# Optimization experiments

Measured on AMD Instinct MI355X. Metric: run time of the kernel, lower is better.

## Reference

```python
import jax, jax.numpy as jnp
import numpy as np

INPUT_WIDTH = 256
DEPTH = 7
OUTPUT_WIDTH = 256
N_NODES = 2 ** (DEPTH + 1) - 1  # 255


def setup_inputs() -> dict:
    key = jax.random.key(0)
    k_x, k_w1, k_w2 = jax.random.split(key, 3)
    init1 = 1.0 / np.sqrt(INPUT_WIDTH)
    x = jax.random.normal(k_x, (2, 1024, INPUT_WIDTH), dtype=jnp.float32)
    w1s = jax.random.uniform(k_w1, (N_NODES, INPUT_WIDTH), jnp.float32, -init1, init1)
    b1s = jnp.zeros((N_NODES,), jnp.float32)
    w2s = jax.random.uniform(k_w2, (N_NODES, INPUT_WIDTH, OUTPUT_WIDTH), jnp.float32, -init1, init1)
    b2s = jnp.zeros((N_NODES, OUTPUT_WIDTH), jnp.float32)
    return {"x": x, "w1s": w1s, "b1s": b1s, "w2s": w2s, "b2s": b2s}


def reference(x, w1s, b1s, w2s, b2s):
    B, S, D = x.shape
    flat_x = x.reshape(B * S, D)  # [T, D]
    T = flat_x.shape[0]

    # --- routing pass: walk the binary tree, recording node ids and logits ---
    current = jnp.zeros((T,), dtype=jnp.int32)
    all_nodes = []
    all_logits = []
    for _ in range(DEPTH + 1):
        all_nodes.append(current)
        score = jnp.einsum('td,td->t', flat_x, w1s[current]) + b1s[current]  # [T]
        all_logits.append(score)
        # ((sign+1)/2).long(): sign(0)->0 maps to choice 0 via truncation
        choice = ((jnp.sign(score) + 1.0) / 2.0).astype(jnp.int32)
        current = current * 2 + choice + 1

    logits = jnp.stack(all_logits, axis=1)  # [T, DEPTH+1]
    path_weights = jax.nn.gelu(jnp.abs(logits), approximate=False)  # exact erf GELU

    # --- output pass: weighted sum of per-node transforms along the path ---
    out = jnp.zeros((T, OUTPUT_WIDTH), dtype=x.dtype)
    for i in range(DEPTH + 1):
        nodes_i = all_nodes[i]
        t_i = jnp.einsum('td,tdo->to', flat_x, w2s[nodes_i]) + b2s[nodes_i]  # [T, O]
        out = out + t_i * path_weights[:, i][:, None]

    return out.reshape(B, S, OUTPUT_WIDTH)
```

## Files before the change

kernel.cpp:

```cpp
#include <hip/hip_runtime.h>
#include <hip/hip_bf16.h>

#define T_TOKENS 2048
#define DIM 256
#define NLEV 8

using bf16x8 = __attribute__((ext_vector_type(8))) short;
using f32x4  = __attribute__((ext_vector_type(4))) float;

__device__ __forceinline__ unsigned short f2bf(float f) {
    union { float f; unsigned u; } v; v.f = f;
    unsigned r = v.u + 0x7FFFu + ((v.u >> 16) & 1u);
    return (unsigned short)(r >> 16);
}

__global__ __launch_bounds__(256) void route_kernel(
    const float* __restrict__ x, const float* __restrict__ w1s,
    const float* __restrict__ b1s,
    float* __restrict__ pw,
    int*   __restrict__ pc,
    unsigned short* __restrict__ xbf)
{
    int wave = threadIdx.x >> 6;
    int lane = threadIdx.x & 63;
    int t = blockIdx.x * 4 + wave;

    const float4 xv = *reinterpret_cast<const float4*>(x + (size_t)t * DIM + lane * 4);

    ushort4 xb;
    xb.x = f2bf(xv.x); xb.y = f2bf(xv.y); xb.z = f2bf(xv.z); xb.w = f2bf(xv.w);
    *reinterpret_cast<ushort4*>(xbf + (size_t)t * DIM + lane * 4) = xb;

    int p = 1;
    float keep = 0.0f;
    #pragma unroll
    for (int lvl = 0; lvl < NLEV; ++lvl) {
        int node = p - 1;
        const float4 wv = *reinterpret_cast<const float4*>(w1s + (size_t)node * DIM + lane * 4);
        float s = xv.x * wv.x + xv.y * wv.y + xv.z * wv.z + xv.w * wv.w;
        #pragma unroll
        for (int off = 32; off; off >>= 1) s += __shfl_xor(s, off);
        float score = s + b1s[node];
        float a = fabsf(score);
        float g = a * 0.5f * (1.0f + erff(a * 0.70710678118654752f));
        if (lane == lvl) keep = g;
        int choice = (score > 0.0f) ? 1 : 0;
        p = 2 * p + choice;
    }
    if (lane < NLEV) pw[(size_t)t * NLEV + lane] = keep;
    if (lane == 0) pc[t] = p;
}

__global__ __launch_bounds__(256) void sort_kernel(
    const int* __restrict__ pc,
    int* __restrict__ order, unsigned* __restrict__ units, int* __restrict__ ucount)
{
    __shared__ int hist[256];
    __shared__ int offs[256];
    __shared__ int cums[257];
    __shared__ int wpart[4];
    int tid = threadIdx.x;
    hist[tid] = 0;
    __syncthreads();

    int myPc[8];
    #pragma unroll
    for (int i = 0; i < 8; ++i) {
        int t = tid * 8 + i;
        myPc[i] = pc[t];
        atomicAdd(&hist[myPc[i] - 256], 1);
    }
    __syncthreads();

    if (tid < 64) {
        int lane = tid;
        int v0 = hist[lane * 4 + 0], v1 = hist[lane * 4 + 1];
        int v2 = hist[lane * 4 + 2], v3 = hist[lane * 4 + 3];
        int sum = v0 + v1 + v2 + v3;
        int scan = sum;
        #pragma unroll
        for (int off = 1; off < 64; off <<= 1) {
            int n = __shfl_up(scan, off);
            if (lane >= off) scan += n;
        }
        int excl = scan - sum;
        offs[lane * 4 + 0] = excl;
        offs[lane * 4 + 1] = excl + v0;
        offs[lane * 4 + 2] = excl + v0 + v1;
        offs[lane * 4 + 3] = excl + v0 + v1 + v2;
    }
    __syncthreads();

    cums[tid] = offs[tid];
    if (tid == 0) cums[256] = T_TOKENS;
    __syncthreads();

    #pragma unroll
    for (int i = 0; i < 8; ++i) {
        int t = tid * 8 + i;
        int bin = myPc[i] - 256;
        int pos = atomicAdd(&offs[bin], 1);
        order[pos] = t;
    }

    int nch = 0, s = 0, e = 0, l = 0;
    if (tid < 255) {
        int q = tid + 1;
        l = 31 - __clz(q);
        int shift = 8 - l;
        int lo = (q << shift) - 256;
        int hi = ((q + 1) << shift) - 256;
        s = cums[lo];
        e = cums[hi];
        nch = (e - s + 63) >> 6;
    }
    int lane = tid & 63, w = tid >> 6;
    int scan = nch;
    #pragma unroll
    for (int off = 1; off < 64; off <<= 1) {
        int n = __shfl_up(scan, off);
        if (lane >= off) scan += n;
    }
    if (lane == 63) wpart[w] = scan;
    __syncthreads();
    int pre = 0;
    for (int k = 0; k < w; ++k) pre += wpart[k];
    int base = pre + scan - nch;
    for (int j = 0; j < nch; ++j) {
        int st = s + j * 64;
        int c = e - st; if (c > 64) c = 64;
        units[base + j] = (unsigned)tid | ((unsigned)l << 8) |
                          ((unsigned)st << 11) | ((unsigned)c << 22);
    }
    if (tid == 255) *ucount = pre + scan;
}

__global__ __launch_bounds__(256, 2) void out_kernel(
    const unsigned short* __restrict__ xbf, const float* __restrict__ w2s,
    const float* __restrict__ b2s, const float* __restrict__ pw,
    const int* __restrict__ order, const unsigned* __restrict__ units,
    const int* __restrict__ ucount, float* __restrict__ lvlbuf)
{
    int u = blockIdx.x >> 2;
    if (u >= *ucount) return;
    unsigned d = units[u];
    int node  = (int)(d & 255u);
    int lvl   = (int)((d >> 8) & 7u);
    int start = (int)((d >> 11) & 2047u);
    int cnt   = (int)((d >> 22) & 127u);

    int wv = threadIdx.x >> 6, lane = threadIdx.x & 63;
    int strip = (blockIdx.x & 3) * 4 + wv;
    int colbase = strip * 16;
    int l15 = lane & 15, kg = lane >> 4;

    int tok[4];
    #pragma unroll
    for (int m = 0; m < 4; ++m) {
        int r = m * 16 + l15;
        tok[m] = order[start + (r < cnt ? r : cnt - 1)];
    }

    const float* w2n = w2s + ((size_t)node << 16) + colbase + l15;
    bf16x8 bfr[8];
    #pragma unroll
    for (int ks = 0; ks < 8; ++ks) {
        const float* bp = w2n + (size_t)(ks * 32 + kg * 8) * DIM;
        float t0 = bp[0 * DIM], t1 = bp[1 * DIM], t2 = bp[2 * DIM], t3 = bp[3 * DIM];
        float t4 = bp[4 * DIM], t5 = bp[5 * DIM], t6 = bp[6 * DIM], t7 = bp[7 * DIM];
        bf16x8 v;
        v[0] = (short)f2bf(t0); v[1] = (short)f2bf(t1);
        v[2] = (short)f2bf(t2); v[3] = (short)f2bf(t3);
        v[4] = (short)f2bf(t4); v[5] = (short)f2bf(t5);
        v[6] = (short)f2bf(t6); v[7] = (short)f2bf(t7);
        bfr[ks] = v;
    }

    float bias = b2s[((size_t)node << 8) + colbase + l15];
    float* dst = lvlbuf + ((size_t)lvl << 19);
    int nmt = (cnt + 15) >> 4;

    bf16x8 aA[8], aB[8];
    auto loadA = [&](int m, bf16x8 (&a)[8]) {
        const unsigned short* xp = xbf + ((size_t)tok[m] << 8) + kg * 8;
        #pragma unroll
        for (int ks = 0; ks < 8; ++ks)
            a[ks] = *reinterpret_cast<const bf16x8*>(xp + ks * 32);
    };
    auto tile = [&](int m, const bf16x8 (&a)[8]) {
        f32x4 acc = {0.f, 0.f, 0.f, 0.f};
        #pragma unroll
        for (int ks = 0; ks < 8; ++ks)
            acc = __builtin_amdgcn_mfma_f32_16x16x32_bf16(a[ks], bfr[ks], acc, 0, 0, 0);
        #pragma unroll
        for (int j = 0; j < 4; ++j) {
            int r = m * 16 + kg * 4 + j;
            if (r < cnt) {
                int t = __shfl(tok[m], kg * 4 + j);
                float w = pw[(size_t)t * NLEV + lvl];
                dst[((size_t)t << 8) + colbase + l15] = w * (acc[j] + bias);
            }
        }
    };

    loadA(0, aA);
    if (nmt > 1) {
        loadA(1, aB);
        tile(0, aA);
        if (nmt > 2) {
            loadA(2, aA);
            tile(1, aB);
            if (nmt > 3) {
                loadA(3, aB);
                tile(2, aA);
                tile(3, aB);
            } else {
                tile(2, aA);
            }
        } else {
            tile(1, aB);
        }
    } else {
        tile(0, aA);
    }
}

__global__ __launch_bounds__(256) void reduce_kernel(
    const float* __restrict__ lvlbuf, float* __restrict__ out)
{
    int idx = blockIdx.x * 256 + threadIdx.x;
    const float4* lb = reinterpret_cast<const float4*>(lvlbuf);
    float4 s = lb[idx];
    #pragma unroll
    for (int l = 1; l < NLEV; ++l) {
        float4 v = lb[(size_t)l * 131072 + idx];
        s.x += v.x; s.y += v.y; s.z += v.z; s.w += v.w;
    }
    reinterpret_cast<float4*>(out)[idx] = s;
}

extern "C" void kernel_launch(void* const* d_in, const int* in_sizes, int n_in,
                              void* d_out, int out_size, void* d_ws, size_t ws_size,
                              hipStream_t stream) {
    const float* x   = (const float*)d_in[0];
    const float* w1s = (const float*)d_in[1];
    const float* b1s = (const float*)d_in[2];
    const float* w2s = (const float*)d_in[3];
    const float* b2s = (const float*)d_in[4];
    float* out = (float*)d_out;

    float* pw            = (float*)d_ws;
    int* pc              = (int*)(pw + T_TOKENS * NLEV);
    int* order           = pc + T_TOKENS;
    unsigned* units      = (unsigned*)(order + T_TOKENS);
    int* ucount          = (int*)(units + 512);
    unsigned short* xbf  = (unsigned short*)((char*)d_ws + (256 << 10));
    float* lvlbuf        = (float*)((char*)d_ws + (2 << 20));

    route_kernel<<<T_TOKENS / 4, 256, 0, stream>>>(x, w1s, b1s, pw, pc, xbf);
    sort_kernel<<<1, 256, 0, stream>>>(pc, order, units, ucount);
    out_kernel<<<2048, 256, 0, stream>>>(xbf, w2s, b2s, pw, order, units, ucount, lvlbuf);
    reduce_kernel<<<512, 256, 0, stream>>>(lvlbuf, out);
}
```

Before: 49.86 us.

## Pre-convert w2s to transposed bf16 in fused routing kernel for coalesced loads

Adds conversion blocks to the routing kernel that transpose every node's w2 matrix into a column-major bf16 buffer through LDS. The output kernel then loads B fragments as contiguous 16-byte vectors instead of strided fp32 scalar loads with per-element conversion. This removes the strided access pattern and conversion work in the GEMM kernel, but adds a full read of all weights plus a write and re-read of a 33MB bf16 copy every call.

```diff
diff --git a/kernel.cpp b/kernel.cpp
--- a/kernel.cpp
+++ b/kernel.cpp
@@ -4,6 +4,7 @@
 #define T_TOKENS 2048
 #define DIM 256
 #define NLEV 8
+#define NCONV 4080
 
 using bf16x8 = __attribute__((ext_vector_type(8))) short;
 using f32x4  = __attribute__((ext_vector_type(4))) float;
@@ -14,16 +15,44 @@
     return (unsigned short)(r >> 16);
 }
 
-__global__ __launch_bounds__(256) void route_kernel(
+__global__ __launch_bounds__(256) void fused_kernel(
     const float* __restrict__ x, const float* __restrict__ w1s,
-    const float* __restrict__ b1s,
-    float* __restrict__ pw,
-    int*   __restrict__ pc,
-    unsigned short* __restrict__ xbf)
-{
+    const float* __restrict__ b1s, const float* __restrict__ w2s,
+    float* __restrict__ pw, int* __restrict__ pc,
+    unsigned short* __restrict__ xbf, unsigned short* __restrict__ w2bfT)
+{
+    __shared__ unsigned short ldsT[64][80];
+
+    if (blockIdx.x < NCONV) {
+        int node = blockIdx.x >> 4;
+        int tile = blockIdx.x & 15;
+        int k0 = (tile >> 2) * 64, c0 = (tile & 3) * 64;
+        const float* src = w2s + ((size_t)node << 16);
+        int tid = threadIdx.x;
+        int rb = tid >> 4, c4 = tid & 15;
+        #pragma unroll
+        for (int i = 0; i < 4; ++i) {
+            int row = rb + i * 16;
+            float4 v = *reinterpret_cast<const float4*>(src + (size_t)(k0 + row) * 256 + c0 + c4 * 4);
+            ldsT[c4 * 4 + 0][row] = f2bf(v.x);
+            ldsT[c4 * 4 + 1][row] = f2bf(v.y);
+            ldsT[c4 * 4 + 2][row] = f2bf(v.z);
+            ldsT[c4 * 4 + 3][row] = f2bf(v.w);
+        }
+        __syncthreads();
+        int c = tid >> 2, ko = (tid & 3) * 16;
+        unsigned short* dst = w2bfT + ((size_t)node << 16) + (size_t)(c0 + c) * 256 + k0 + ko;
+        uint4 t0 = *reinterpret_cast<const uint4*>(&ldsT[c][ko]);
+        uint4 t1 = *reinterpret_cast<const uint4*>(&ldsT[c][ko + 8]);
+        *reinterpret_cast<uint4*>(dst)     = t0;
+        *reinterpret_cast<uint4*>(dst + 8) = t1;
+        return;
+    }
+
+    int bid = blockIdx.x - NCONV;
     int wave = threadIdx.x >> 6;
     int lane = threadIdx.x & 63;
-    int t = blockIdx.x * 4 + wave;
+    int t = bid * 4 + wave;
 
     const float4 xv = *reinterpret_cast<const float4*>(x + (size_t)t * DIM + lane * 4);
 
@@ -136,7 +165,7 @@
 }
 
 __global__ __launch_bounds__(256, 2) void out_kernel(
-    const unsigned short* __restrict__ xbf, const float* __restrict__ w2s,
+    const unsigned short* __restrict__ xbf, const unsigned short* __restrict__ w2bfT,
     const float* __restrict__ b2s, const float* __restrict__ pw,
     const int* __restrict__ order, const unsigned* __restrict__ units,
     const int* __restrict__ ucount, float* __restrict__ lvlbuf)
@@ -161,20 +190,11 @@
         tok[m] = order[start + (r < cnt ? r : cnt - 1)];
     }
 
-    const float* w2n = w2s + ((size_t)node << 16) + colbase + l15;
+    const unsigned short* w2c = w2bfT + ((size_t)node << 16) + (size_t)(colbase + l15) * 256 + kg * 8;
     bf16x8 bfr[8];
     #pragma unroll
-    for (int ks = 0; ks < 8; ++ks) {
-        const float* bp = w2n + (size_t)(ks * 32 + kg * 8) * DIM;
-        float t0 = bp[0 * DIM], t1 = bp[1 * DIM], t2 = bp[2 * DIM], t3 = bp[3 * DIM];
-        float t4 = bp[4 * DIM], t5 = bp[5 * DIM], t6 = bp[6 * DIM], t7 = bp[7 * DIM];
-        bf16x8 v;
-        v[0] = (short)f2bf(t0); v[1] = (short)f2bf(t1);
-        v[2] = (short)f2bf(t2); v[3] = (short)f2bf(t3);
-        v[4] = (short)f2bf(t4); v[5] = (short)f2bf(t5);
-        v[6] = (short)f2bf(t6); v[7] = (short)f2bf(t7);
-        bfr[ks] = v;
-    }
+    for (int ks = 0; ks < 8; ++ks)
+        bfr[ks] = *reinterpret_cast<const bf16x8*>(w2c + ks * 32);
 
     float bias = b2s[((size_t)node << 8) + colbase + l15];
     float* dst = lvlbuf + ((size_t)lvl << 19);
@@ -249,16 +269,17 @@
     const float* b2s = (const float*)d_in[4];
     float* out = (float*)d_out;
 
-    float* pw            = (float*)d_ws;
-    int* pc              = (int*)(pw + T_TOKENS * NLEV);
-    int* order           = pc + T_TOKENS;
-    unsigned* units      = (unsigned*)(order + T_TOKENS);
-    int* ucount          = (int*)(units + 512);
-    unsigned short* xbf  = (unsigned short*)((char*)d_ws + (256 << 10));
-    float* lvlbuf        = (float*)((char*)d_ws + (2 << 20));
-
-    route_kernel<<<T_TOKENS / 4, 256, 0, stream>>>(x, w1s, b1s, pw, pc, xbf);
+    float* pw             = (float*)d_ws;
+    int* pc               = (int*)(pw + T_TOKENS * NLEV);
+    int* order            = pc + T_TOKENS;
+    unsigned* units       = (unsigned*)(order + T_TOKENS);
+    int* ucount           = (int*)(units + 512);
+    unsigned short* xbf   = (unsigned short*)((char*)d_ws + (256 << 10));
+    float* lvlbuf         = (float*)((char*)d_ws + (2 << 20));
+    unsigned short* w2bfT = (unsigned short*)((char*)d_ws + ((size_t)32 << 20));
+
+    fused_kernel<<<NCONV + 512, 256, 0, stream>>>(x, w1s, b1s, w2s, pw, pc, xbf, w2bfT);
     sort_kernel<<<1, 256, 0, stream>>>(pc, order, units, ucount);
-    out_kernel<<<2048, 256, 0, stream>>>(xbf, w2s, b2s, pw, order, units, ucount, lvlbuf);
+    out_kernel<<<2048, 256, 0, stream>>>(xbf, w2bfT, b2s, pw, order, units, ucount, lvlbuf);
     reduce_kernel<<<512, 256, 0, stream>>>(lvlbuf, out);
 }
```

Measured after the change: 64.61 us. 1.3x slower.

## Use 256-token work units with single-wave blocks covering 32 columns each

Applied to the files above, without the earlier changes.

Work units now hold up to 256 tokens instead of 64, so nodes high in the tree are split into far fewer units and each node's weight slice is loaded and converted fewer times. Each block becomes a single 64-thread wave that computes a 32-column strip with two MFMA accumulators and loops over all 16-row tiles. Block IDs are remapped so the eight strips of the same unit are spread across the grid. The cost is less parallelism per unit and the loss of the explicit double-buffered A loads, so the large top-level units now run long serial loops.

```diff
diff --git a/kernel.cpp b/kernel.cpp
--- a/kernel.cpp
+++ b/kernel.cpp
@@ -4,6 +4,7 @@
 #define T_TOKENS 2048
 #define DIM 256
 #define NLEV 8
+#define MAXU 320
 
 using bf16x8 = __attribute__((ext_vector_type(8))) short;
 using f32x4  = __attribute__((ext_vector_type(4))) float;
@@ -112,7 +113,7 @@
         int hi = ((q + 1) << shift) - 256;
         s = cums[lo];
         e = cums[hi];
-        nch = (e - s + 63) >> 6;
+        nch = (e - s + 255) >> 8;
     }
     int lane = tid & 63, w = tid >> 6;
     int scan = nch;
@@ -127,101 +128,89 @@
     for (int k = 0; k < w; ++k) pre += wpart[k];
     int base = pre + scan - nch;
     for (int j = 0; j < nch; ++j) {
-        int st = s + j * 64;
-        int c = e - st; if (c > 64) c = 64;
+        int st = s + j * 256;
+        int c = e - st; if (c > 256) c = 256;
         units[base + j] = (unsigned)tid | ((unsigned)l << 8) |
-                          ((unsigned)st << 11) | ((unsigned)c << 22);
+                          ((unsigned)st << 11) | ((unsigned)(c - 1) << 22);
     }
     if (tid == 255) *ucount = pre + scan;
 }
 
-__global__ __launch_bounds__(256, 2) void out_kernel(
+__global__ __launch_bounds__(64, 4) void out_kernel(
     const unsigned short* __restrict__ xbf, const float* __restrict__ w2s,
     const float* __restrict__ b2s, const float* __restrict__ pw,
     const int* __restrict__ order, const unsigned* __restrict__ units,
     const int* __restrict__ ucount, float* __restrict__ lvlbuf)
 {
-    int u = blockIdx.x >> 2;
+    int bid = blockIdx.x;
+    int L = (bid & 7) * MAXU + (bid >> 3);
+    int u = L >> 3, strip = L & 7;
     if (u >= *ucount) return;
     unsigned d = units[u];
     int node  = (int)(d & 255u);
     int lvl   = (int)((d >> 8) & 7u);
     int start = (int)((d >> 11) & 2047u);
-    int cnt   = (int)((d >> 22) & 127u);
-
-    int wv = threadIdx.x >> 6, lane = threadIdx.x & 63;
-    int strip = (blockIdx.x & 3) * 4 + wv;
-    int colbase = strip * 16;
+    int cnt   = (int)((d >> 22) & 255u) + 1;
+
+    int lane = threadIdx.x;
     int l15 = lane & 15, kg = lane >> 4;
-
-    int tok[4];
-    #pragma unroll
-    for (int m = 0; m < 4; ++m) {
-        int r = m * 16 + l15;
-        tok[m] = order[start + (r < cnt ? r : cnt - 1)];
-    }
+    int colbase = strip * 32;
+
+    int i1 = 64 + lane, i2 = 128 + lane, i3 = 192 + lane;
+    int ord0 = order[start + (lane < cnt ? lane : cnt - 1)];
+    int ord1 = order[start + (i1 < cnt ? i1 : cnt - 1)];
+    int ord2 = order[start + (i2 < cnt ? i2 : cnt - 1)];
+    int ord3 = order[start + (i3 < cnt ? i3 : cnt - 1)];
 
     const float* w2n = w2s + ((size_t)node << 16) + colbase + l15;
-    bf16x8 bfr[8];
+    bf16x8 bfr0[8], bfr1[8];
     #pragma unroll
     for (int ks = 0; ks < 8; ++ks) {
         const float* bp = w2n + (size_t)(ks * 32 + kg * 8) * DIM;
-        float t0 = bp[0 * DIM], t1 = bp[1 * DIM], t2 = bp[2 * DIM], t3 = bp[3 * DIM];
-        float t4 = bp[4 * DIM], t5 = bp[5 * DIM], t6 = bp[6 * DIM], t7 = bp[7 * DIM];
-        bf16x8 v;
-        v[0] = (short)f2bf(t0); v[1] = (short)f2bf(t1);
-        v[2] = (short)f2bf(t2); v[3] = (short)f2bf(t3);
-        v[4] = (short)f2bf(t4); v[5] = (short)f2bf(t5);
-        v[6] = (short)f2bf(t6); v[7] = (short)f2bf(t7);
-        bfr[ks] = v;
-    }
-
-    float bias = b2s[((size_t)node << 8) + colbase + l15];
+        bf16x8 v0, v1;
+        #pragma unroll
+        for (int i = 0; i < 8; ++i) {
+            v0[i] = (short)f2bf(bp[(size_t)i * DIM]);
+            v1[i] = (short)f2bf(bp[(size_t)i * DIM + 16]);
+        }
+        bfr0[ks] = v0;
+        bfr1[ks] = v1;
+    }
+
+    float bias0 = b2s[((size_t)node << 8) + colbase + l15];
+    float bias1 = b2s[((size_t)node << 8) + colbase + 16 + l15];
     float* dst = lvlbuf + ((size_t)lvl << 19);
     int nmt = (cnt + 15) >> 4;
 
-    bf16x8 aA[8], aB[8];
-    auto loadA = [&](int m, bf16x8 (&a)[8]) {
-        const unsigned short* xp = xbf + ((size_t)tok[m] << 8) + kg * 8;
+    for (int m = 0; m < nmt; ++m) {
+        int sel = m >> 2;
+        int vsrc = (sel == 0) ? ord0 : (sel == 1) ? ord1 : (sel == 2) ? ord2 : ord3;
+        int tk = __shfl(vsrc, (m & 3) * 16 + l15);
+
+        const unsigned short* xp = xbf + ((size_t)tk << 8) + kg * 8;
+        bf16x8 a[8];
         #pragma unroll
         for (int ks = 0; ks < 8; ++ks)
             a[ks] = *reinterpret_cast<const bf16x8*>(xp + ks * 32);
-    };
-    auto tile = [&](int m, const bf16x8 (&a)[8]) {
-        f32x4 acc = {0.f, 0.f, 0.f, 0.f};
-        #pragma unroll
-        for (int ks = 0; ks < 8; ++ks)
-            acc = __builtin_amdgcn_mfma_f32_16x16x32_bf16(a[ks], bfr[ks], acc, 0, 0, 0);
+
+        f32x4 acc0 = {0.f, 0.f, 0.f, 0.f};
+        f32x4 acc1 = {0.f, 0.f, 0.f, 0.f};
+        #pragma unroll
+        for (int ks = 0; ks < 8; ++ks) {
+            acc0 = __builtin_amdgcn_mfma_f32_16x16x32_bf16(a[ks], bfr0[ks], acc0, 0, 0, 0);
+            acc1 = __builtin_amdgcn_mfma_f32_16x16x32_bf16(a[ks], bfr1[ks], acc1, 0, 0, 0);
+        }
+
         #pragma unroll
         for (int j = 0; j < 4; ++j) {
             int r = m * 16 + kg * 4 + j;
             if (r < cnt) {
-                int t = __shfl(tok[m], kg * 4 + j);
+                int t = __shfl(tk, kg * 4 + j);
                 float w = pw[(size_t)t * NLEV + lvl];
-                dst[((size_t)t << 8) + colbase + l15] = w * (acc[j] + bias);
+                dst[((size_t)t << 8) + colbase + l15]      = w * (acc0[j] + bias0);
+                dst[((size_t)t << 8) + colbase + 16 + l15] = w * (acc1[j] + bias1);
             }
         }
-    };
-
-    loadA(0, aA);
-    if (nmt > 1) {
-        loadA(1, aB);
-        tile(0, aA);
-        if (nmt > 2) {
-            loadA(2, aA);
-            tile(1, aB);
-            if (nmt > 3) {
-                loadA(3, aB);
-                tile(2, aA);
-                tile(3, aB);
-            } else {
-                tile(2, aA);
-            }
-        } else {
-            tile(1, aB);
-        }
-    } else {
-        tile(0, aA);
     }
 }
 
@@ -259,6 +248,6 @@
 
     route_kernel<<<T_TOKENS / 4, 256, 0, stream>>>(x, w1s, b1s, pw, pc, xbf);
     sort_kernel<<<1, 256, 0, stream>>>(pc, order, units, ucount);
-    out_kernel<<<2048, 256, 0, stream>>>(xbf, w2s, b2s, pw, order, units, ucount, lvlbuf);
+    out_kernel<<<8 * MAXU, 64, 0, stream>>>(xbf, w2s, b2s, pw, order, units, ucount, lvlbuf);
     reduce_kernel<<<512, 256, 0, stream>>>(lvlbuf, out);
 }
```

After: 71.78 us. +43.9%, slower.

## Stage W2 tiles through LDS with async double-buffered loads in out_kernel

Applied to the files above, without the earlier changes.

Restructures out_kernel so each unit uses 2 blocks of 128 columns instead of 4 blocks of 64. W2 fp32 rows are streamed into double-buffered shared memory with global_load_lds and converted to bf16 when read from LDS. K-steps are pipelined with barriers while activation fragments are prefetched. This aims to get coalesced weight loads and overlap memory with MFMA, at the cost of LDS usage, more barriers and fewer blocks.

```diff
diff --git a/kernel.cpp b/kernel.cpp
--- a/kernel.cpp
+++ b/kernel.cpp
@@ -4,6 +4,7 @@
 #define T_TOKENS 2048
 #define DIM 256
 #define NLEV 8
+#define MAXU 512
 
 using bf16x8 = __attribute__((ext_vector_type(8))) short;
 using f32x4  = __attribute__((ext_vector_type(4))) float;
@@ -17,8 +18,7 @@
 __global__ __launch_bounds__(256) void route_kernel(
     const float* __restrict__ x, const float* __restrict__ w1s,
     const float* __restrict__ b1s,
-    float* __restrict__ pw,
-    int*   __restrict__ pc,
+    float* __restrict__ pw, int* __restrict__ pc,
     unsigned short* __restrict__ xbf)
 {
     int wave = threadIdx.x >> 6;
@@ -135,23 +135,25 @@
     if (tid == 255) *ucount = pre + scan;
 }
 
-__global__ __launch_bounds__(256, 2) void out_kernel(
+__global__ __launch_bounds__(256, 4) void out_kernel(
     const unsigned short* __restrict__ xbf, const float* __restrict__ w2s,
     const float* __restrict__ b2s, const float* __restrict__ pw,
     const int* __restrict__ order, const unsigned* __restrict__ units,
     const int* __restrict__ ucount, float* __restrict__ lvlbuf)
 {
-    int u = blockIdx.x >> 2;
+    __shared__ float Bs[2][32][128];
+
+    int u = blockIdx.x >> 1;
     if (u >= *ucount) return;
     unsigned d = units[u];
     int node  = (int)(d & 255u);
     int lvl   = (int)((d >> 8) & 7u);
     int start = (int)((d >> 11) & 2047u);
     int cnt   = (int)((d >> 22) & 127u);
-
-    int wv = threadIdx.x >> 6, lane = threadIdx.x & 63;
-    int strip = (blockIdx.x & 3) * 4 + wv;
-    int colbase = strip * 16;
+    int ch = blockIdx.x & 1;
+
+    int tid = threadIdx.x;
+    int wv = tid >> 6, lane = tid & 63;
     int l15 = lane & 15, kg = lane >> 4;
 
     int tok[4];
@@ -161,67 +163,96 @@
         tok[m] = order[start + (r < cnt ? r : cnt - 1)];
     }
 
-    const float* w2n = w2s + ((size_t)node << 16) + colbase + l15;
-    bf16x8 bfr[8];
-    #pragma unroll
-    for (int ks = 0; ks < 8; ++ks) {
-        const float* bp = w2n + (size_t)(ks * 32 + kg * 8) * DIM;
-        float t0 = bp[0 * DIM], t1 = bp[1 * DIM], t2 = bp[2 * DIM], t3 = bp[3 * DIM];
-        float t4 = bp[4 * DIM], t5 = bp[5 * DIM], t6 = bp[6 * DIM], t7 = bp[7 * DIM];
-        bf16x8 v;
-        v[0] = (short)f2bf(t0); v[1] = (short)f2bf(t1);
-        v[2] = (short)f2bf(t2); v[3] = (short)f2bf(t3);
-        v[4] = (short)f2bf(t4); v[5] = (short)f2bf(t5);
-        v[6] = (short)f2bf(t6); v[7] = (short)f2bf(t7);
-        bfr[ks] = v;
-    }
-
-    float bias = b2s[((size_t)node << 8) + colbase + l15];
+    const float* w2n = w2s + ((size_t)node << 16) + ch * 128;
+    int srow = wv * 8 + (lane >> 5);
+    int scol = (lane & 31) * 4;
+
+    auto STAGE = [&](int p, int q) {
+        #pragma unroll
+        for (int i = 0; i < 4; ++i) {
+            const float* src = w2n + (size_t)(p * 32 + srow + i * 2) * 256 + scol;
+            float* dst = &Bs[q][wv * 8 + i * 2][0];
+            __builtin_amdgcn_global_load_lds(
+                (const __attribute__((address_space(1))) void*)src,
+                (__attribute__((address_space(3))) void*)dst, 16, 0, 0);
+        }
+    };
+    auto LOADA = [&](int p, bf16x8 (&a)[4]) {
+        #pragma unroll
+        for (int m = 0; m < 4; ++m)
+            a[m] = *reinterpret_cast<const bf16x8*>(xbf + ((size_t)tok[m] << 8) + p * 32 + kg * 8);
+    };
+
+    f32x4 acc[4][2];
+    #pragma unroll
+    for (int m = 0; m < 4; ++m) {
+        acc[m][0] = (f32x4){0.f, 0.f, 0.f, 0.f};
+        acc[m][1] = (f32x4){0.f, 0.f, 0.f, 0.f};
+    }
+
+    auto COMPUTE = [&](int q, const bf16x8 (&a)[4]) {
+        bf16x8 bf[2];
+        #pragma unroll
+        for (int nb = 0; nb < 2; ++nb) {
+            bf16x8 v;
+            #pragma unroll
+            for (int i = 0; i < 8; ++i)
+                v[i] = (short)f2bf(Bs[q][kg * 8 + i][wv * 32 + nb * 16 + l15]);
+            bf[nb] = v;
+        }
+        #pragma unroll
+        for (int m = 0; m < 4; ++m) if (m * 16 < cnt)
+            #pragma unroll
+            for (int nb = 0; nb < 2; ++nb)
+                acc[m][nb] = __builtin_amdgcn_mfma_f32_16x16x32_bf16(a[m], bf[nb], acc[m][nb], 0, 0, 0);
+    };
+
+    bf16x8 aP[4], aQ[4];
+
+    STAGE(0, 0);
+    LOADA(0, aP);
+    STAGE(1, 1);
+    asm volatile("s_waitcnt vmcnt(4)" ::: "memory");
+    __builtin_amdgcn_s_barrier();
+    __builtin_amdgcn_sched_barrier(0);
+
+    #pragma unroll
+    for (int p = 0; p < 8; ++p) {
+        if (p & 1) COMPUTE(1, aQ); else COMPUTE(0, aP);
+        __builtin_amdgcn_s_barrier();
+        if (p < 6) {
+            if (p & 1) LOADA(p + 1, aP); else LOADA(p + 1, aQ);
+            STAGE(p + 2, p & 1);
+            asm volatile("s_waitcnt vmcnt(4)" ::: "memory");
+        } else if (p == 6) {
+            LOADA(7, aQ);
+            asm volatile("s_waitcnt vmcnt(0)" ::: "memory");
+        }
+        __builtin_amdgcn_s_barrier();
+        __builtin_amdgcn_sched_barrier(0);
+    }
+
+    float bias[2];
+    #pragma unroll
+    for (int nb = 0; nb < 2; ++nb)
+        bias[nb] = b2s[((size_t)node << 8) + ch * 128 + wv * 32 + nb * 16 + l15];
+
     float* dst = lvlbuf + ((size_t)lvl << 19);
-    int nmt = (cnt + 15) >> 4;
-
-    bf16x8 aA[8], aB[8];
-    auto loadA = [&](int m, bf16x8 (&a)[8]) {
-        const unsigned short* xp = xbf + ((size_t)tok[m] << 8) + kg * 8;
-        #pragma unroll
-        for (int ks = 0; ks < 8; ++ks)
-            a[ks] = *reinterpret_cast<const bf16x8*>(xp + ks * 32);
-    };
-    auto tile = [&](int m, const bf16x8 (&a)[8]) {
-        f32x4 acc = {0.f, 0.f, 0.f, 0.f};
-        #pragma unroll
-        for (int ks = 0; ks < 8; ++ks)
-            acc = __builtin_amdgcn_mfma_f32_16x16x32_bf16(a[ks], bfr[ks], acc, 0, 0, 0);
+
+    #pragma unroll
+    for (int m = 0; m < 4; ++m) if (m * 16 < cnt) {
         #pragma unroll
         for (int j = 0; j < 4; ++j) {
             int r = m * 16 + kg * 4 + j;
             if (r < cnt) {
                 int t = __shfl(tok[m], kg * 4 + j);
                 float w = pw[(size_t)t * NLEV + lvl];
-                dst[((size_t)t << 8) + colbase + l15] = w * (acc[j] + bias);
+                #pragma unroll
+                for (int nb = 0; nb < 2; ++nb)
+                    dst[((size_t)t << 8) + ch * 128 + wv * 32 + nb * 16 + l15] =
+                        w * (acc[m][nb][j] + bias[nb]);
             }
         }
-    };
-
-    loadA(0, aA);
-    if (nmt > 1) {
-        loadA(1, aB);
-        tile(0, aA);
-        if (nmt > 2) {
-            loadA(2, aA);
-            tile(1, aB);
-            if (nmt > 3) {
-                loadA(3, aB);
-                tile(2, aA);
-                tile(3, aB);
-            } else {
-                tile(2, aA);
-            }
-        } else {
-            tile(1, aB);
-        }
-    } else {
-        tile(0, aA);
     }
 }
 
@@ -253,12 +284,12 @@
     int* pc              = (int*)(pw + T_TOKENS * NLEV);
     int* order           = pc + T_TOKENS;
     unsigned* units      = (unsigned*)(order + T_TOKENS);
-    int* ucount          = (int*)(units + 512);
+    int* ucount          = (int*)(units + MAXU);
     unsigned short* xbf  = (unsigned short*)((char*)d_ws + (256 << 10));
     float* lvlbuf        = (float*)((char*)d_ws + (2 << 20));
 
     route_kernel<<<T_TOKENS / 4, 256, 0, stream>>>(x, w1s, b1s, pw, pc, xbf);
     sort_kernel<<<1, 256, 0, stream>>>(pc, order, units, ucount);
-    out_kernel<<<2048, 256, 0, stream>>>(xbf, w2s, b2s, pw, order, units, ucount, lvlbuf);
+    out_kernel<<<2 * MAXU, 256, 0, stream>>>(xbf, w2s, b2s, pw, order, units, ucount, lvlbuf);
     reduce_kernel<<<512, 256, 0, stream>>>(lvlbuf, out);
 }
```

After: 45.38 us. -9.0%, faster.
